# Performance work log

Measured on AMD Instinct MI355X. Metric: run time of the kernel, lower is better.

The kernel has to match this reference:

```python
import jax, jax.numpy as jnp
import numpy as np

B, S, IN = 64, 600, 3
H, C, K = 512, 80, 20
U = 64  # char_len
OUT = 1 + 6 * K


def lstm_cell(x, h, c, W_ih, W_hh, b_ih, b_hh):
    # PyTorch LSTMCell: gates order i, f, g, o
    gates = x @ W_ih.T + b_ih + h @ W_hh.T + b_hh
    i, f, g, o = jnp.split(gates, 4, axis=1)
    i = jax.nn.sigmoid(i)
    f = jax.nn.sigmoid(f)
    g = jnp.tanh(g)
    o = jax.nn.sigmoid(o)
    c_new = f * c + i * g
    h_new = o * jnp.tanh(c_new)
    return h_new, c_new


def setup_inputs() -> dict:
    key = jax.random.key(0)
    ks = jax.random.split(key, 16)
    sc = 0.05
    return {
        "x": jax.random.normal(ks[0], (B, S, IN), jnp.float32),
        "chars": jax.random.uniform(ks[1], (B, U, C), jnp.float32),
        "W_ih1": jax.random.normal(ks[2], (4 * H, IN + C), jnp.float32) * sc,
        "W_hh1": jax.random.normal(ks[3], (4 * H, H), jnp.float32) * sc,
        "b_ih1": jnp.zeros((4 * H,), jnp.float32),
        "b_hh1": jnp.zeros((4 * H,), jnp.float32),
        "W_win": jax.random.normal(ks[4], (3 * K, H), jnp.float32) * sc,
        "b_win": jnp.zeros((3 * K,), jnp.float32),
        "W_ih2": jax.random.normal(ks[5], (4 * H, IN + C), jnp.float32) * sc,
        "W_hh2": jax.random.normal(ks[6], (4 * H, H), jnp.float32) * sc,
        "b_ih2": jnp.zeros((4 * H,), jnp.float32),
        "b_hh2": jnp.zeros((4 * H,), jnp.float32),
        "W_mdn": jax.random.normal(ks[7], (OUT, H), jnp.float32) * sc,
        "b_mdn": jnp.zeros((OUT,), jnp.float32),
    }


def reference(x, chars, W_ih1, W_hh1, b_ih1, b_hh1, W_win, b_win,
              W_ih2, W_hh2, b_ih2, b_hh2, W_mdn, b_mdn):
    u = jnp.arange(U, dtype=x.dtype)[None, None, :]  # [1,1,U]

    def step(carry, pt):
        h1, c1, h2, c2, window, kappa_prev = carry
        inp1 = jnp.concatenate([pt, window], axis=1)           # [B, IN+C]
        h1, c1 = lstm_cell(inp1, h1, c1, W_ih1, W_hh1, b_ih1, b_hh1)
        # Gaussian window attention (Graves)
        wout = h1 @ W_win.T + b_win                            # [B, 3K]
        a, b_, k = jnp.split(wout, 3, axis=1)
        alpha = jnp.exp(a)[:, :, None]                         # [B,K,1]
        beta = jnp.exp(b_)[:, :, None]
        kappa = kappa_prev + jnp.exp(k)                        # [B,K]
        phi = jnp.sum(alpha * jnp.exp(-beta * (kappa[:, :, None] - u) ** 2), axis=1)  # [B,U]
        window = jnp.einsum('bu,buc->bc', phi, chars)          # [B,C]
        inp2 = jnp.concatenate([pt, window], axis=1)
        h2, c2 = lstm_cell(inp2, h2, c2, W_ih2, W_hh2, b_ih2, b_hh2)
        return (h1, c1, h2, c2, window, kappa), h2

    z = jnp.zeros((B, H), x.dtype)
    carry0 = (z, z, z, z, jnp.zeros((B, C), x.dtype), jnp.zeros((B, K), x.dtype))
    _, hs2 = jax.lax.scan(step, carry0, jnp.transpose(x, (1, 0, 2)))  # [S,B,H]
    outputs = jnp.transpose(hs2, (1, 0, 2)).reshape(-1, H)             # [B*S,H]
    mdn = outputs @ W_mdn.T + b_mdn                                     # [B*S,OUT]

    eos = jax.nn.sigmoid(mdn[:, 0]).reshape(-1, 1)
    pi, mu1, mu2, sigma1, sigma2, rho = jnp.split(mdn[:, 1:], 6, axis=1)
    pi = jax.nn.softmax(pi, axis=1)
    sigma1 = jnp.exp(sigma1)
    sigma2 = jnp.exp(sigma2)
    rho = jnp.tanh(rho)
    return eos, pi, mu1, mu2, sigma1, sigma2, rho
```

## Files before the change

### kernel.cpp

```cpp
#include <hip/hip_runtime.h>


typedef unsigned int u32;
typedef unsigned short u16;
typedef unsigned long long u64;
typedef short short8 __attribute__((ext_vector_type(8)));
typedef float floatx4 __attribute__((ext_vector_type(4)));
typedef u32 u32x4 __attribute__((ext_vector_type(4)));

#define NBLK   193
#define NGEMM  128
#define AGG_BID 192
#define NTHR   512
#define SLEN   600

#define OFF_FLAG 0ull
#define OFF_GEN  16384ull
#define OFF_H1P  32768ull
#define OFF_H2P  (OFF_H1P + 131072ull)
#define OFF_WP   (OFF_H2P + 131072ull)
#define OFF_XHI  (OFF_WP + 24576ull)
#define OFF_XLO  (OFF_XHI + 2457600ull)
#define OFF_HS2  (OFF_XLO + 2457600ull)
#define WS_NEED  (OFF_HS2 + 39321600ull)

__device__ __forceinline__ float bf2f(short h) {
  return __uint_as_float(((u32)(u16)h) << 16);
}
__device__ __forceinline__ u16 f2bf(float f) {
  u32 u = __float_as_uint(f);
  u += 0x7fffu + ((u >> 16) & 1u);
  return (u16)(u >> 16);
}
__device__ __forceinline__ float fsig(float x) { return 1.0f / (1.0f + __expf(-x)); }
__device__ __forceinline__ float ftanh_(float x) { return 2.0f / (1.0f + __expf(-2.0f * x)) - 1.0f; }

__device__ __forceinline__ float lstm_point(floatx4 g, float& c) {
  float i  = fsig(g[0]);
  float f  = fsig(g[1]);
  float gg = ftanh_(g[2]);
  float o  = fsig(g[3]);
  c = f * c + i * gg;
  return o * ftanh_(c);
}

__device__ __forceinline__ u32 pack_split(float v) {
  u32 b = __float_as_uint(v);
  float rem = v - __uint_as_float(b & 0xffff0000u);
  return (b >> 16) | ((u32)f2bf(rem) << 16);
}

__device__ __forceinline__ void st_coh(u32* p, u32 v) {
  __hip_atomic_store(p, v, __ATOMIC_RELAXED, __HIP_MEMORY_SCOPE_AGENT);
}
__device__ __forceinline__ u32 ld_coh(const u32* p) {
  return __hip_atomic_load((u32*)p, __ATOMIC_RELAXED, __HIP_MEMORY_SCOPE_AGENT);
}

__device__ __forceinline__ void ld_pk8(const u32* p, short8& hi, short8& lo) {
  u64 d0 = __hip_atomic_load((u64*)(p + 0), __ATOMIC_RELAXED, __HIP_MEMORY_SCOPE_AGENT);
  u64 d1 = __hip_atomic_load((u64*)(p + 2), __ATOMIC_RELAXED, __HIP_MEMORY_SCOPE_AGENT);
  u64 d2 = __hip_atomic_load((u64*)(p + 4), __ATOMIC_RELAXED, __HIP_MEMORY_SCOPE_AGENT);
  u64 d3 = __hip_atomic_load((u64*)(p + 6), __ATOMIC_RELAXED, __HIP_MEMORY_SCOPE_AGENT);
  u32 a0 = (u32)d0, a1 = (u32)(d0 >> 32), a2 = (u32)d1, a3 = (u32)(d1 >> 32);
  u32 a4 = (u32)d2, a5 = (u32)(d2 >> 32), a6 = (u32)d3, a7 = (u32)(d3 >> 32);
  u32x4 h, l;
  h[0] = __builtin_amdgcn_perm(a1, a0, 0x05040100u); l[0] = __builtin_amdgcn_perm(a1, a0, 0x07060302u);
  h[1] = __builtin_amdgcn_perm(a3, a2, 0x05040100u); l[1] = __builtin_amdgcn_perm(a3, a2, 0x07060302u);
  h[2] = __builtin_amdgcn_perm(a5, a4, 0x05040100u); l[2] = __builtin_amdgcn_perm(a5, a4, 0x07060302u);
  h[3] = __builtin_amdgcn_perm(a7, a6, 0x05040100u); l[3] = __builtin_amdgcn_perm(a7, a6, 0x07060302u);
  hi = __builtin_bit_cast(short8, h);
  lo = __builtin_bit_cast(short8, l);
}

__device__ __forceinline__ void sync_wait(u32* flags, u32* gen, u32 lgen, int bid) {
  if (bid == AGG_BID) {
    const int i = threadIdx.x;
    if (i < NBLK) {
      u32 sp = 0;
      while (ld_coh(&flags[i * 16]) < lgen) {
        __builtin_amdgcn_s_sleep(1);
        if (++sp > (1u << 22)) break;
      }
    }
    __syncthreads();
    if (threadIdx.x < 8) st_coh(&gen[threadIdx.x * 16], lgen);
  } else {
    if (threadIdx.x == 0) {
      u32 sp = 0;
      while (ld_coh(&gen[(bid & 7) * 16]) < lgen) {
        __builtin_amdgcn_s_sleep(2);
        if (++sp > (1u << 22)) break;
      }
    }
  }
}

__device__ __forceinline__ void sync_light(u32* flags, u32* gen, u32& lgen, int bid) {
  asm volatile("s_waitcnt vmcnt(0) lgkmcnt(0)" ::: "memory");
  __syncthreads();
  lgen++;
  if (threadIdx.x == 0) st_coh(&flags[bid * 16], lgen);
  sync_wait(flags, gen, lgen, bid);
  __syncthreads();
  asm volatile("" ::: "memory");
}

__device__ __forceinline__ void sync_full(u32* flags, u32* gen, u32& lgen, int bid) {
  __syncthreads();
  lgen++;
  if (threadIdx.x == 0) {
    __threadfence();
    st_coh(&flags[bid * 16], lgen);
  }
  sync_wait(flags, gen, lgen, bid);
  if (threadIdx.x == 0) __threadfence();
  __syncthreads();
  asm volatile("" ::: "memory");
}

__global__ void init_ws(unsigned char* ws) {
  const int gtid = blockIdx.x * 256 + threadIdx.x;
  u32* flg = (u32*)(ws + OFF_FLAG);
  for (int i = gtid; i < NBLK * 16; i += 64 * 256) flg[i] = 0u;
  u32* gn = (u32*)(ws + OFF_GEN);
  if (gtid < 128) gn[gtid] = 0u;
  u32* h2p = (u32*)(ws + OFF_H2P);
  for (int i = gtid; i < 64 * 512; i += 64 * 256) h2p[i] = 0u;
  u32* wp = (u32*)(ws + OFF_WP);
  for (int i = gtid; i < 64 * 96; i += 64 * 256) wp[i] = 0u;
}

__global__ __launch_bounds__(NTHR, 1) void rnn_kernel(
    const float* __restrict__ x, const float* __restrict__ chars,
    const float* __restrict__ Wih1, const float* __restrict__ Whh1,
    const float* __restrict__ bih1, const float* __restrict__ bhh1,
    const float* __restrict__ Wwin, const float* __restrict__ bwin,
    const float* __restrict__ Wih2, const float* __restrict__ Whh2,
    const float* __restrict__ bih2, const float* __restrict__ bhh2,
    const float* __restrict__ Wmdn, const float* __restrict__ bmdn,
    float* __restrict__ out, unsigned char* __restrict__ ws)
{
  const int bid = blockIdx.x;
  const int tid = threadIdx.x;
  const int wid = tid >> 6;
  const int lane = tid & 63;
  const int unit = wid >> 2;

  u32* flags = (u32*)(ws + OFF_FLAG);
  u32* gen   = (u32*)(ws + OFF_GEN);
  u32* h1p   = (u32*)(ws + OFF_H1P);
  u32* h2p   = (u32*)(ws + OFF_H2P);
  u32* wp    = (u32*)(ws + OFF_WP);
  u16* xhi   = (u16*)(ws + OFF_XHI);
  u16* xlo   = (u16*)(ws + OFF_XLO);
  u16* hs2   = (u16*)(ws + OFF_HS2);

  u32 lgen = 0;

  __shared__ __align__(16) u16 hifrag_s[40 * 512];
  __shared__ __align__(16) u16 lofrag_s[40 * 512];
  __shared__ __align__(16) floatx4 plds[2][256];
  __shared__ __align__(16) float chars_s[64 * 80];
  __shared__ __align__(16) float smem_f[512];
  __shared__ float wout_s[64];
  __shared__ float al_s[20], be_s[20], kp_s[20];

  for (int i = bid * NTHR + tid; i < SLEN * 64 * 32; i += NBLK * NTHR) {
    int t = i >> 11;
    int r = i & 2047;
    int bb = r >> 5, q = r & 31;
    float v = (q < 3) ? x[((size_t)bb * SLEN + t) * 3 + q] : 0.0f;
    u32 b = __float_as_uint(v);
    xhi[i] = (u16)(b >> 16);
    xlo[i] = f2bf(v - __uint_as_float(b & 0xffff0000u));
  }

  const bool isg = (bid < NGEMM);
  const bool isw = (bid >= NGEMM && bid < NGEMM + 64);

  floatx4 bs1v = {0.f,0.f,0.f,0.f}, bs2v = bs1v;
  float c1 = 0.0f, c2 = 0.0f;
  int b_row = 0, hc = 0;
  float bw = 0.0f;
  const int kg = (lane >> 4) * 8;

  if (isg) {
    b_row = 16 * (wid & 3) + (lane & 15);
    hc = 4 * bid + (lane >> 4);
    if (wid == 0) {
      const int ra = lane & 15;
      const int origA = (ra & 3) * 512 + 4 * bid + (ra >> 2);
      #pragma unroll
      for (int ks = 0; ks < 20; ++ks) {
        short8 v1h, v1l, v2h, v2l;
        #pragma unroll
        for (int j = 0; j < 8; ++j) {
          int k = 32 * ks + kg + j;
          float a1 = 0.0f, a2 = 0.0f;
          if (k < 512) {
            a1 = Whh1[(size_t)origA * 512 + k];
            a2 = Whh2[(size_t)origA * 512 + k];
          } else if (k < 592) {
            a1 = Wih1[(size_t)origA * 83 + 3 + (k - 512)];
            a2 = Wih2[(size_t)origA * 83 + 3 + (k - 512)];
          } else if (k >= 608 && k < 611) {
            a1 = Wih1[(size_t)origA * 83 + (k - 608)];
            a2 = Wih2[(size_t)origA * 83 + (k - 608)];
          }
          u32 b1 = __float_as_uint(a1), b2 = __float_as_uint(a2);
          v1h[j] = (short)(u16)(b1 >> 16);
          v2h[j] = (short)(u16)(b2 >> 16);
          v1l[j] = (short)f2bf(a1 - __uint_as_float(b1 & 0xffff0000u));
          v2l[j] = (short)f2bf(a2 - __uint_as_float(b2 & 0xffff0000u));
        }
        *(short8*)(hifrag_s + ((0 * 20 + ks) << 9) + (lane << 3)) = v1h;
        *(short8*)(hifrag_s + ((1 * 20 + ks) << 9) + (lane << 3)) = v2h;
        *(short8*)(lofrag_s + ((0 * 20 + ks) << 9) + (lane << 3)) = v1l;
        *(short8*)(lofrag_s + ((1 * 20 + ks) << 9) + (lane << 3)) = v2l;
      }
    }
    #pragma unroll
    for (int r = 0; r < 4; ++r) {
      bs1v[r] = bih1[r * 512 + hc] + bhh1[r * 512 + hc];
      bs2v[r] = bih2[r * 512 + hc] + bhh2[r * 512 + hc];
    }
  } else if (isw) {
    const int b = bid - NGEMM;
    for (int i = tid; i < 64 * 80; i += NTHR)
      chars_s[i] = chars[(size_t)b * 5120 + i];
    if (tid < 20) kp_s[tid] = 0.0f;
    if (tid < 60) bw = bwin[tid];
  }

  sync_full(flags, gen, lgen, bid);

  if (isg) {
    if (unit == 0) {
      floatx4 a = {0.f,0.f,0.f,0.f}, b = a, c = a;
      short8 xh = *(const short8*)(xhi + (size_t)b_row * 32 + kg);
      short8 xl = *(const short8*)(xlo + (size_t)b_row * 32 + kg);
      short8 ah = *(const short8*)(hifrag_s + (19 << 9) + (lane << 3));
      short8 al = *(const short8*)(lofrag_s + (19 << 9) + (lane << 3));
      a = __builtin_amdgcn_mfma_f32_16x16x32_bf16(ah, xh, a, 0, 0, 0);
      b = __builtin_amdgcn_mfma_f32_16x16x32_bf16(ah, xl, b, 0, 0, 0);
      c = __builtin_amdgcn_mfma_f32_16x16x32_bf16(al, xh, c, 0, 0, 0);
      plds[0][tid] = a + b + c;
    }
    __syncthreads();
    if (unit == 1) {
      floatx4 g = plds[0][tid - 256] + bs1v;
      float h = lstm_point(g, c1);
      st_coh(&h1p[b_row * 512 + hc], pack_split(h));
    }
  }

  sync_light(flags, gen, lgen, bid);

  for (int t = 0; t < SLEN; ++t) {
    floatx4 a1a = {0.f,0.f,0.f,0.f}, a1b = a1a, a1c = a1a;
    floatx4 a2a = {0.f,0.f,0.f,0.f}, a2b = a2a, a2c = a2a;

    if (isg) {
      if (unit == 0) {
        {
          floatx4 pa = {0.f,0.f,0.f,0.f}, pb = pa, pc = pa;
          short8 bh[8], bl[8];
          #pragma unroll
          for (int k = 0; k < 8; ++k)
            ld_pk8(h2p + b_row * 512 + k * 32 + kg, bh[k], bl[k]);
          #pragma unroll
          for (int k = 0; k < 8; ++k) {
            short8 ah = *(const short8*)(hifrag_s + ((20 + k) << 9) + (lane << 3));
            short8 al = *(const short8*)(lofrag_s + ((20 + k) << 9) + (lane << 3));
            pa = __builtin_amdgcn_mfma_f32_16x16x32_bf16(ah, bh[k], pa, 0, 0, 0);
            pb = __builtin_amdgcn_mfma_f32_16x16x32_bf16(ah, bl[k], pb, 0, 0, 0);
            pc = __builtin_amdgcn_mfma_f32_16x16x32_bf16(al, bh[k], pc, 0, 0, 0);
          }
          short8 xh = *(const short8*)(xhi + ((size_t)t * 64 + b_row) * 32 + kg);
          short8 xl = *(const short8*)(xlo + ((size_t)t * 64 + b_row) * 32 + kg);
          short8 ah = *(const short8*)(hifrag_s + ((20 + 19) << 9) + (lane << 3));
          short8 al = *(const short8*)(lofrag_s + ((20 + 19) << 9) + (lane << 3));
          pa = __builtin_amdgcn_mfma_f32_16x16x32_bf16(ah, xh, pa, 0, 0, 0);
          pb = __builtin_amdgcn_mfma_f32_16x16x32_bf16(ah, xl, pb, 0, 0, 0);
          pc = __builtin_amdgcn_mfma_f32_16x16x32_bf16(al, xh, pc, 0, 0, 0);
          plds[1][tid] = pa + pb + pc;
        }
        if (t < SLEN - 1) {
          floatx4 pa = {0.f,0.f,0.f,0.f}, pb = pa, pc = pa;
          short8 bh[8], bl[8];
          #pragma unroll
          for (int k = 0; k < 8; ++k)
            ld_pk8(h1p + b_row * 512 + k * 32 + kg, bh[k], bl[k]);
          #pragma unroll
          for (int k = 0; k < 8; ++k) {
            short8 ah = *(const short8*)(hifrag_s + (k << 9) + (lane << 3));
            short8 al = *(const short8*)(lofrag_s + (k << 9) + (lane << 3));
            pa = __builtin_amdgcn_mfma_f32_16x16x32_bf16(ah, bh[k], pa, 0, 0, 0);
            pb = __builtin_amdgcn_mfma_f32_16x16x32_bf16(ah, bl[k], pb, 0, 0, 0);
            pc = __builtin_amdgcn_mfma_f32_16x16x32_bf16(al, bh[k], pc, 0, 0, 0);
          }
          short8 xh = *(const short8*)(xhi + ((size_t)(t + 1) * 64 + b_row) * 32 + kg);
          short8 xl = *(const short8*)(xlo + ((size_t)(t + 1) * 64 + b_row) * 32 + kg);
          short8 ah = *(const short8*)(hifrag_s + (19 << 9) + (lane << 3));
          short8 al = *(const short8*)(lofrag_s + (19 << 9) + (lane << 3));
          pa = __builtin_amdgcn_mfma_f32_16x16x32_bf16(ah, xh, pa, 0, 0, 0);
          pb = __builtin_amdgcn_mfma_f32_16x16x32_bf16(ah, xl, pb, 0, 0, 0);
          pc = __builtin_amdgcn_mfma_f32_16x16x32_bf16(al, xh, pc, 0, 0, 0);
          plds[0][tid] = pa + pb + pc;
        }
      } else {
        {
          short8 bh[8], bl[8];
          #pragma unroll
          for (int k = 0; k < 8; ++k)
            ld_pk8(h2p + b_row * 512 + (8 + k) * 32 + kg, bh[k], bl[k]);
          #pragma unroll
          for (int k = 0; k < 8; ++k) {
            short8 ah = *(const short8*)(hifrag_s + ((20 + 8 + k) << 9) + (lane << 3));
            short8 al = *(const short8*)(lofrag_s + ((20 + 8 + k) << 9) + (lane << 3));
            a2a = __builtin_amdgcn_mfma_f32_16x16x32_bf16(ah, bh[k], a2a, 0, 0, 0);
            a2b = __builtin_amdgcn_mfma_f32_16x16x32_bf16(ah, bl[k], a2b, 0, 0, 0);
            a2c = __builtin_amdgcn_mfma_f32_16x16x32_bf16(al, bh[k], a2c, 0, 0, 0);
          }
        }
        if (t < SLEN - 1) {
          short8 bh[8], bl[8];
          #pragma unroll
          for (int k = 0; k < 8; ++k)
            ld_pk8(h1p + b_row * 512 + (8 + k) * 32 + kg, bh[k], bl[k]);
          #pragma unroll
          for (int k = 0; k < 8; ++k) {
            short8 ah = *(const short8*)(hifrag_s + ((8 + k) << 9) + (lane << 3));
            short8 al = *(const short8*)(lofrag_s + ((8 + k) << 9) + (lane << 3));
            a1a = __builtin_amdgcn_mfma_f32_16x16x32_bf16(ah, bh[k], a1a, 0, 0, 0);
            a1b = __builtin_amdgcn_mfma_f32_16x16x32_bf16(ah, bl[k], a1b, 0, 0, 0);
            a1c = __builtin_amdgcn_mfma_f32_16x16x32_bf16(al, bh[k], a1c, 0, 0, 0);
          }
        }
      }
    } else if (isw) {
      const int b = bid - NGEMM;
      {
        u32 p = ld_coh(&h1p[b * 512 + tid]);
        smem_f[tid] = bf2f((short)(u16)p) + bf2f((short)(u16)(p >> 16));
      }
      __syncthreads();
      const int col = tid & 63;
      const int kq  = tid >> 6;
      float p = 0.0f;
      if (col < 60) {
        const floatx4* wr = (const floatx4*)(Wwin + (size_t)col * 512 + kq * 64);
        const floatx4* hr = (const floatx4*)(smem_f + kq * 64);
        #pragma unroll
        for (int k4 = 0; k4 < 16; ++k4) {
          floatx4 wv = wr[k4];
          floatx4 hv = hr[k4];
          p = fmaf(wv[0], hv[0], p);
          p = fmaf(wv[1], hv[1], p);
          p = fmaf(wv[2], hv[2], p);
          p = fmaf(wv[3], hv[3], p);
        }
      }
      __syncthreads();
      smem_f[tid] = p;
      __syncthreads();
      if (tid < 60) {
        float s = 0.0f;
        #pragma unroll
        for (int q = 0; q < 8; ++q) s += smem_f[q * 64 + tid];
        wout_s[tid] = s + bw;
      }
      __syncthreads();
      if (tid < 20) {
        al_s[tid] = __expf(wout_s[tid]);
        be_s[tid] = __expf(wout_s[20 + tid]);
        kp_s[tid] += __expf(wout_s[40 + tid]);
      }
      __syncthreads();
      if (tid < 64) {
        float u = (float)tid;
        float ph = 0.0f;
        #pragma unroll
        for (int k = 0; k < 20; ++k) {
          float d = kp_s[k] - u;
          ph = fmaf(al_s[k], __expf(-be_s[k] * d * d), ph);
        }
        smem_f[tid] = ph;
      }
      __syncthreads();
      if (tid < 80) {
        float wv = 0.0f;
        for (int u = 0; u < 64; ++u)
          wv = fmaf(smem_f[u], chars_s[u * 80 + tid], wv);
        st_coh(&wp[b * 96 + tid], pack_split(wv));
      }
    }

    sync_light(flags, gen, lgen, bid);

    if (isg && unit == 1) {
      const int j = tid - 256;
      short8 wh0, wl0, wh1, wl1, wh2, wl2;
      ld_pk8(wp + b_row * 96 +  0 + kg, wh0, wl0);
      ld_pk8(wp + b_row * 96 + 32 + kg, wh1, wl1);
      ld_pk8(wp + b_row * 96 + 64 + kg, wh2, wl2);
      {
        short8 ah0 = *(const short8*)(hifrag_s + ((20 + 16) << 9) + (lane << 3));
        short8 ah1 = *(const short8*)(hifrag_s + ((20 + 17) << 9) + (lane << 3));
        short8 ah2 = *(const short8*)(hifrag_s + ((20 + 18) << 9) + (lane << 3));
        short8 al0 = *(const short8*)(lofrag_s + ((20 + 16) << 9) + (lane << 3));
        short8 al1 = *(const short8*)(lofrag_s + ((20 + 17) << 9) + (lane << 3));
        short8 al2 = *(const short8*)(lofrag_s + ((20 + 18) << 9) + (lane << 3));
        a2a = __builtin_amdgcn_mfma_f32_16x16x32_bf16(ah0, wh0, a2a, 0, 0, 0);
        a2b = __builtin_amdgcn_mfma_f32_16x16x32_bf16(ah0, wl0, a2b, 0, 0, 0);
        a2c = __builtin_amdgcn_mfma_f32_16x16x32_bf16(al0, wh0, a2c, 0, 0, 0);
        a2a = __builtin_amdgcn_mfma_f32_16x16x32_bf16(ah1, wh1, a2a, 0, 0, 0);
        a2b = __builtin_amdgcn_mfma_f32_16x16x32_bf16(ah1, wl1, a2b, 0, 0, 0);
        a2c = __builtin_amdgcn_mfma_f32_16x16x32_bf16(al1, wh1, a2c, 0, 0, 0);
        a2a = __builtin_amdgcn_mfma_f32_16x16x32_bf16(ah2, wh2, a2a, 0, 0, 0);
        a2b = __builtin_amdgcn_mfma_f32_16x16x32_bf16(ah2, wl2, a2b, 0, 0, 0);
        a2c = __builtin_amdgcn_mfma_f32_16x16x32_bf16(al2, wh2, a2c, 0, 0, 0);
      }
      floatx4 g2 = a2a + a2b + a2c + plds[1][j] + bs2v;
      float h2v = lstm_point(g2, c2);
      st_coh(&h2p[b_row * 512 + hc], pack_split(h2v));
      hs2[((size_t)b_row * SLEN + t) * 512 + hc] = f2bf(h2v);
      if (t < SLEN - 1) {
        short8 ah0 = *(const short8*)(hifrag_s + (16 << 9) + (lane << 3));
        short8 ah1 = *(const short8*)(hifrag_s + (17 << 9) + (lane << 3));
        short8 ah2 = *(const short8*)(hifrag_s + (18 << 9) + (lane << 3));
        short8 al0 = *(const short8*)(lofrag_s + (16 << 9) + (lane << 3));
        short8 al1 = *(const short8*)(lofrag_s + (17 << 9) + (lane << 3));
        short8 al2 = *(const short8*)(lofrag_s + (18 << 9) + (lane << 3));
        a1a = __builtin_amdgcn_mfma_f32_16x16x32_bf16(ah0, wh0, a1a, 0, 0, 0);
        a1b = __builtin_amdgcn_mfma_f32_16x16x32_bf16(ah0, wl0, a1b, 0, 0, 0);
        a1c = __builtin_amdgcn_mfma_f32_16x16x32_bf16(al0, wh0, a1c, 0, 0, 0);
        a1a = __builtin_amdgcn_mfma_f32_16x16x32_bf16(ah1, wh1, a1a, 0, 0, 0);
        a1b = __builtin_amdgcn_mfma_f32_16x16x32_bf16(ah1, wl1, a1b, 0, 0, 0);
        a1c = __builtin_amdgcn_mfma_f32_16x16x32_bf16(al1, wh1, a1c, 0, 0, 0);
        a1a = __builtin_amdgcn_mfma_f32_16x16x32_bf16(ah2, wh2, a1a, 0, 0, 0);
        a1b = __builtin_amdgcn_mfma_f32_16x16x32_bf16(ah2, wl2, a1b, 0, 0, 0);
        a1c = __builtin_amdgcn_mfma_f32_16x16x32_bf16(al2, wh2, a1c, 0, 0, 0);
        floatx4 g1 = a1a + a1b + a1c + plds[0][j] + bs1v;
        float h1v = lstm_point(g1, c1);
        st_coh(&h1p[b_row * 512 + hc], pack_split(h1v));
      }
    }

    sync_light(flags, gen, lgen, bid);
  }

  sync_full(flags, gen, lgen, bid);

  {
    const int row = bid * NTHR + tid;
    if (row < 38400) {
      const u16* hrow = hs2 + (size_t)row * 512;
      {
        float acc = bmdn[0];
        for (int k8 = 0; k8 < 512; k8 += 8) {
          short8 hv = *(const short8*)(hrow + k8);
          #pragma unroll
          for (int j = 0; j < 8; ++j) acc = fmaf(bf2f(hv[j]), Wmdn[k8 + j], acc);
        }
        out[row] = fsig(acc);
      }
      {
        float a[20];
        #pragma unroll
        for (int cc = 0; cc < 20; ++cc) a[cc] = bmdn[1 + cc];
        for (int k8 = 0; k8 < 512; k8 += 8) {
          short8 hv = *(const short8*)(hrow + k8);
          float hf[8];
          #pragma unroll
          for (int j = 0; j < 8; ++j) hf[j] = bf2f(hv[j]);
          #pragma unroll
          for (int cc = 0; cc < 20; ++cc) {
            const float* wr = Wmdn + (size_t)(1 + cc) * 512 + k8;
            #pragma unroll
            for (int j = 0; j < 8; ++j) a[cc] = fmaf(hf[j], wr[j], a[cc]);
          }
        }
        float mx = a[0];
        #pragma unroll
        for (int cc = 1; cc < 20; ++cc) mx = fmaxf(mx, a[cc]);
        float s = 0.0f;
        #pragma unroll
        for (int cc = 0; cc < 20; ++cc) { a[cc] = __expf(a[cc] - mx); s += a[cc]; }
        float inv = 1.0f / s;
        float* po = out + 38400 + (size_t)row * 20;
        #pragma unroll
        for (int cc = 0; cc < 20; ++cc) po[cc] = a[cc] * inv;
      }
      for (int grp = 1; grp <= 5; ++grp) {
        float a[20];
        #pragma unroll
        for (int cc = 0; cc < 20; ++cc) a[cc] = bmdn[1 + 20 * grp + cc];
        for (int k8 = 0; k8 < 512; k8 += 8) {
          short8 hv = *(const short8*)(hrow + k8);
          float hf[8];
          #pragma unroll
          for (int j = 0; j < 8; ++j) hf[j] = bf2f(hv[j]);
          #pragma unroll
          for (int cc = 0; cc < 20; ++cc) {
            const float* wr = Wmdn + (size_t)(1 + 20 * grp + cc) * 512 + k8;
            #pragma unroll
            for (int j = 0; j < 8; ++j) a[cc] = fmaf(hf[j], wr[j], a[cc]);
          }
        }
        float* po = out + 38400 + (size_t)grp * 768000 + (size_t)row * 20;
        if (grp == 3 || grp == 4) {
          #pragma unroll
          for (int cc = 0; cc < 20; ++cc) po[cc] = __expf(a[cc]);
        } else if (grp == 5) {
          #pragma unroll
          for (int cc = 0; cc < 20; ++cc) po[cc] = ftanh_(a[cc]);
        } else {
          #pragma unroll
          for (int cc = 0; cc < 20; ++cc) po[cc] = a[cc];
        }
      }
    }
  }
}

extern "C" void kernel_launch(void* const* d_in, const int* in_sizes, int n_in,
                              void* d_out, int out_size, void* d_ws, size_t ws_size,
                              hipStream_t stream) {
  (void)in_sizes; (void)n_in; (void)out_size;
  if (ws_size < WS_NEED) return;
  init_ws<<<dim3(64), dim3(256), 0, stream>>>((unsigned char*)d_ws);
  rnn_kernel<<<dim3(NBLK), dim3(NTHR), 0, stream>>>(
      (const float*)d_in[0],  (const float*)d_in[1],
      (const float*)d_in[2],  (const float*)d_in[3],
      (const float*)d_in[4],  (const float*)d_in[5],
      (const float*)d_in[6],  (const float*)d_in[7],
      (const float*)d_in[8],  (const float*)d_in[9],
      (const float*)d_in[10], (const float*)d_in[11],
      (const float*)d_in[12], (const float*)d_in[13],
      (float*)d_out, (unsigned char*)d_ws);
}
```

Before: 12.31 ms.

## Halve GEMM block count, doubling hidden columns per block with register-cached weights

Cuts the GEMM blocks from 128 to 64, so each block now computes 8 hidden columns, split into two groups of 4, instead of 4. The total grid drops from 193 to 129 blocks, which reduces the number of participants in each grid-wide barrier per timestep. To fit the doubled weight set, the layer-1 high-part weight fragments are held in registers per wave and the rest go into one packed LDS buffer. The cost is twice the MFMA work per block per step and higher register pressure, which could lengthen the serial critical path or lower occupancy.

```diff
diff --git a/kernel.cpp b/kernel.cpp
--- a/kernel.cpp
+++ b/kernel.cpp
@@ -8,9 +8,9 @@
 typedef float floatx4 __attribute__((ext_vector_type(4)));
 typedef u32 u32x4 __attribute__((ext_vector_type(4)));
 
-#define NBLK   193
-#define NGEMM  128
-#define AGG_BID 192
+#define NBLK   129
+#define NGEMM  64
+#define AGG_BID 128
 #define NTHR   512
 #define SLEN   600
 
@@ -23,6 +23,11 @@
 #define OFF_XLO  (OFF_XHI + 2457600ull)
 #define OFF_HS2  (OFF_XLO + 2457600ull)
 #define WS_NEED  (OFF_HS2 + 39321600ull)
+
+#define L_LO(m,ks,hcq)  ((((m)*20+(ks))*2+(hcq)) << 10)
+#define L_HI2(ks,hcq)   (81920u + ((((ks)*2+(hcq))) << 10))
+#define L_PLDS(m,hcq)   (122880u + (((m)*2+(hcq)) << 12))
+#define LDS_BYTES 139264u
 
 __device__ __forceinline__ float bf2f(short h) {
   return __uint_as_float(((u32)(u16)h) << 16);
@@ -158,13 +163,13 @@
 
   u32 lgen = 0;
 
-  __shared__ __align__(16) u16 hifrag_s[40 * 512];
-  __shared__ __align__(16) u16 lofrag_s[40 * 512];
-  __shared__ __align__(16) floatx4 plds[2][256];
-  __shared__ __align__(16) float chars_s[64 * 80];
-  __shared__ __align__(16) float smem_f[512];
-  __shared__ float wout_s[64];
-  __shared__ float al_s[20], be_s[20], kp_s[20];
+  __shared__ __align__(16) unsigned char lds_raw[LDS_BYTES];
+  float* chars_s = (float*)lds_raw;
+  float* smem_f  = (float*)(lds_raw + 20480);
+  float* wout_s  = (float*)(lds_raw + 22528);
+  float* al_s    = (float*)(lds_raw + 22784);
+  float* be_s    = (float*)(lds_raw + 22864);
+  float* kp_s    = (float*)(lds_raw + 22944);
 
   for (int i = bid * NTHR + tid; i < SLEN * 64 * 32; i += NBLK * NTHR) {
     int t = i >> 11;
@@ -179,52 +184,77 @@
   const bool isg = (bid < NGEMM);
   const bool isw = (bid >= NGEMM && bid < NGEMM + 64);
 
-  floatx4 bs1v = {0.f,0.f,0.f,0.f}, bs2v = bs1v;
-  float c1 = 0.0f, c2 = 0.0f;
-  int b_row = 0, hc = 0;
+  short8 af1h[2][11];
+  floatx4 bs1q[2] = {{0,0,0,0},{0,0,0,0}}, bs2q[2] = {{0,0,0,0},{0,0,0,0}};
+  float c1q[2] = {0.0f, 0.0f}, c2q[2] = {0.0f, 0.0f};
+  int b_row = 0;
+  int hcv[2] = {0, 0};
   float bw = 0.0f;
   const int kg = (lane >> 4) * 8;
 
   if (isg) {
     b_row = 16 * (wid & 3) + (lane & 15);
-    hc = 4 * bid + (lane >> 4);
+    hcv[0] = 8 * bid + (lane >> 4);
+    hcv[1] = 8 * bid + 4 + (lane >> 4);
+    const int ra = lane & 15;
     if (wid == 0) {
-      const int ra = lane & 15;
-      const int origA = (ra & 3) * 512 + 4 * bid + (ra >> 2);
-      #pragma unroll
-      for (int ks = 0; ks < 20; ++ks) {
-        short8 v1h, v1l, v2h, v2l;
+      #pragma unroll
+      for (int hcq = 0; hcq < 2; ++hcq) {
+        const int origA = (ra & 3) * 512 + 8 * bid + 4 * hcq + (ra >> 2);
+        #pragma unroll
+        for (int ks = 0; ks < 20; ++ks) {
+          short8 v1l, v2h, v2l;
+          #pragma unroll
+          for (int j = 0; j < 8; ++j) {
+            int k = 32 * ks + kg + j;
+            float a1 = 0.0f, a2 = 0.0f;
+            if (k < 512) {
+              a1 = Whh1[(size_t)origA * 512 + k];
+              a2 = Whh2[(size_t)origA * 512 + k];
+            } else if (k < 592) {
+              a1 = Wih1[(size_t)origA * 83 + 3 + (k - 512)];
+              a2 = Wih2[(size_t)origA * 83 + 3 + (k - 512)];
+            } else if (k >= 608 && k < 611) {
+              a1 = Wih1[(size_t)origA * 83 + (k - 608)];
+              a2 = Wih2[(size_t)origA * 83 + (k - 608)];
+            }
+            u32 b1 = __float_as_uint(a1), b2 = __float_as_uint(a2);
+            v2h[j] = (short)(u16)(b2 >> 16);
+            v1l[j] = (short)f2bf(a1 - __uint_as_float(b1 & 0xffff0000u));
+            v2l[j] = (short)f2bf(a2 - __uint_as_float(b2 & 0xffff0000u));
+          }
+          *(short8*)(lds_raw + L_HI2(ks, hcq) + (lane << 4)) = v2h;
+          *(short8*)(lds_raw + L_LO(0, ks, hcq) + (lane << 4)) = v1l;
+          *(short8*)(lds_raw + L_LO(1, ks, hcq) + (lane << 4)) = v2l;
+        }
+      }
+    }
+    #pragma unroll
+    for (int hcq = 0; hcq < 2; ++hcq) {
+      const int origA = (ra & 3) * 512 + 8 * bid + 4 * hcq + (ra >> 2);
+      #pragma unroll
+      for (int s = 0; s < 11; ++s) {
+        int ks = (unit == 0) ? ((s < 8) ? s : 19) : (8 + s);
+        short8 vh;
         #pragma unroll
         for (int j = 0; j < 8; ++j) {
           int k = 32 * ks + kg + j;
-          float a1 = 0.0f, a2 = 0.0f;
-          if (k < 512) {
-            a1 = Whh1[(size_t)origA * 512 + k];
-            a2 = Whh2[(size_t)origA * 512 + k];
-          } else if (k < 592) {
-            a1 = Wih1[(size_t)origA * 83 + 3 + (k - 512)];
-            a2 = Wih2[(size_t)origA * 83 + 3 + (k - 512)];
-          } else if (k >= 608 && k < 611) {
-            a1 = Wih1[(size_t)origA * 83 + (k - 608)];
-            a2 = Wih2[(size_t)origA * 83 + (k - 608)];
-          }
-          u32 b1 = __float_as_uint(a1), b2 = __float_as_uint(a2);
-          v1h[j] = (short)(u16)(b1 >> 16);
-          v2h[j] = (short)(u16)(b2 >> 16);
-          v1l[j] = (short)f2bf(a1 - __uint_as_float(b1 & 0xffff0000u));
-          v2l[j] = (short)f2bf(a2 - __uint_as_float(b2 & 0xffff0000u));
-        }
-        *(short8*)(hifrag_s + ((0 * 20 + ks) << 9) + (lane << 3)) = v1h;
-        *(short8*)(hifrag_s + ((1 * 20 + ks) << 9) + (lane << 3)) = v2h;
-        *(short8*)(lofrag_s + ((0 * 20 + ks) << 9) + (lane << 3)) = v1l;
-        *(short8*)(lofrag_s + ((1 * 20 + ks) << 9) + (lane << 3)) = v2l;
+          float a1 = 0.0f;
+          if (k < 512)                    a1 = Whh1[(size_t)origA * 512 + k];
+          else if (k < 592)               a1 = Wih1[(size_t)origA * 83 + 3 + (k - 512)];
+          else if (k >= 608 && k < 611)   a1 = Wih1[(size_t)origA * 83 + (k - 608)];
+          vh[j] = (short)(u16)(__float_as_uint(a1) >> 16);
+        }
+        af1h[hcq][s] = vh;
       }
     }
     #pragma unroll
-    for (int r = 0; r < 4; ++r) {
-      bs1v[r] = bih1[r * 512 + hc] + bhh1[r * 512 + hc];
-      bs2v[r] = bih2[r * 512 + hc] + bhh2[r * 512 + hc];
-    }
+    for (int hcq = 0; hcq < 2; ++hcq)
+      #pragma unroll
+      for (int r = 0; r < 4; ++r) {
+        bs1q[hcq][r] = bih1[r * 512 + hcv[hcq]] + bhh1[r * 512 + hcv[hcq]];
+        bs2q[hcq][r] = bih2[r * 512 + hcv[hcq]] + bhh2[r * 512 + hcv[hcq]];
+      }
   } else if (isw) {
     const int b = bid - NGEMM;
     for (int i = tid; i < 64 * 80; i += NTHR)
@@ -237,77 +267,95 @@
 
   if (isg) {
     if (unit == 0) {
-      floatx4 a = {0.f,0.f,0.f,0.f}, b = a, c = a;
       short8 xh = *(const short8*)(xhi + (size_t)b_row * 32 + kg);
       short8 xl = *(const short8*)(xlo + (size_t)b_row * 32 + kg);
-      short8 ah = *(const short8*)(hifrag_s + (19 << 9) + (lane << 3));
-      short8 al = *(const short8*)(lofrag_s + (19 << 9) + (lane << 3));
-      a = __builtin_amdgcn_mfma_f32_16x16x32_bf16(ah, xh, a, 0, 0, 0);
-      b = __builtin_amdgcn_mfma_f32_16x16x32_bf16(ah, xl, b, 0, 0, 0);
-      c = __builtin_amdgcn_mfma_f32_16x16x32_bf16(al, xh, c, 0, 0, 0);
-      plds[0][tid] = a + b + c;
+      #pragma unroll
+      for (int hcq = 0; hcq < 2; ++hcq) {
+        floatx4 a = {0.f,0.f,0.f,0.f}, b = a, c = a;
+        short8 ah = af1h[hcq][8];
+        short8 al = *(const short8*)(lds_raw + L_LO(0, 19, hcq) + (lane << 4));
+        a = __builtin_amdgcn_mfma_f32_16x16x32_bf16(ah, xh, a, 0, 0, 0);
+        b = __builtin_amdgcn_mfma_f32_16x16x32_bf16(ah, xl, b, 0, 0, 0);
+        c = __builtin_amdgcn_mfma_f32_16x16x32_bf16(al, xh, c, 0, 0, 0);
+        *(floatx4*)(lds_raw + L_PLDS(0, hcq) + (tid << 4)) = a + b + c;
+      }
     }
     __syncthreads();
     if (unit == 1) {
-      floatx4 g = plds[0][tid - 256] + bs1v;
-      float h = lstm_point(g, c1);
-      st_coh(&h1p[b_row * 512 + hc], pack_split(h));
+      const int j = tid & 255;
+      #pragma unroll
+      for (int hcq = 0; hcq < 2; ++hcq) {
+        floatx4 g = *(const floatx4*)(lds_raw + L_PLDS(0, hcq) + (j << 4)) + bs1q[hcq];
+        float h = lstm_point(g, c1q[hcq]);
+        st_coh(&h1p[b_row * 512 + hcv[hcq]], pack_split(h));
+      }
     }
   }
 
   sync_light(flags, gen, lgen, bid);
 
   for (int t = 0; t < SLEN; ++t) {
-    floatx4 a1a = {0.f,0.f,0.f,0.f}, a1b = a1a, a1c = a1a;
-    floatx4 a2a = {0.f,0.f,0.f,0.f}, a2b = a2a, a2c = a2a;
+    floatx4 a1[2][3], a2[2][3];
+    #pragma unroll
+    for (int hcq = 0; hcq < 2; ++hcq)
+      #pragma unroll
+      for (int m = 0; m < 3; ++m) { a1[hcq][m] = {0.f,0.f,0.f,0.f}; a2[hcq][m] = {0.f,0.f,0.f,0.f}; }
 
     if (isg) {
       if (unit == 0) {
         {
-          floatx4 pa = {0.f,0.f,0.f,0.f}, pb = pa, pc = pa;
           short8 bh[8], bl[8];
           #pragma unroll
           for (int k = 0; k < 8; ++k)
             ld_pk8(h2p + b_row * 512 + k * 32 + kg, bh[k], bl[k]);
           #pragma unroll
-          for (int k = 0; k < 8; ++k) {
-            short8 ah = *(const short8*)(hifrag_s + ((20 + k) << 9) + (lane << 3));
-            short8 al = *(const short8*)(lofrag_s + ((20 + k) << 9) + (lane << 3));
-            pa = __builtin_amdgcn_mfma_f32_16x16x32_bf16(ah, bh[k], pa, 0, 0, 0);
-            pb = __builtin_amdgcn_mfma_f32_16x16x32_bf16(ah, bl[k], pb, 0, 0, 0);
-            pc = __builtin_amdgcn_mfma_f32_16x16x32_bf16(al, bh[k], pc, 0, 0, 0);
-          }
+          for (int k = 0; k < 8; ++k)
+            #pragma unroll
+            for (int hcq = 0; hcq < 2; ++hcq) {
+              short8 ah = *(const short8*)(lds_raw + L_HI2(k, hcq) + (lane << 4));
+              short8 al = *(const short8*)(lds_raw + L_LO(1, k, hcq) + (lane << 4));
+              a2[hcq][0] = __builtin_amdgcn_mfma_f32_16x16x32_bf16(ah, bh[k], a2[hcq][0], 0, 0, 0);
+              a2[hcq][1] = __builtin_amdgcn_mfma_f32_16x16x32_bf16(ah, bl[k], a2[hcq][1], 0, 0, 0);
+              a2[hcq][2] = __builtin_amdgcn_mfma_f32_16x16x32_bf16(al, bh[k], a2[hcq][2], 0, 0, 0);
+            }
           short8 xh = *(const short8*)(xhi + ((size_t)t * 64 + b_row) * 32 + kg);
           short8 xl = *(const short8*)(xlo + ((size_t)t * 64 + b_row) * 32 + kg);
-          short8 ah = *(const short8*)(hifrag_s + ((20 + 19) << 9) + (lane << 3));
-          short8 al = *(const short8*)(lofrag_s + ((20 + 19) << 9) + (lane << 3));
-          pa = __builtin_amdgcn_mfma_f32_16x16x32_bf16(ah, xh, pa, 0, 0, 0);
-          pb = __builtin_amdgcn_mfma_f32_16x16x32_bf16(ah, xl, pb, 0, 0, 0);
-          pc = __builtin_amdgcn_mfma_f32_16x16x32_bf16(al, xh, pc, 0, 0, 0);
-          plds[1][tid] = pa + pb + pc;
+          #pragma unroll
+          for (int hcq = 0; hcq < 2; ++hcq) {
+            short8 ah = *(const short8*)(lds_raw + L_HI2(19, hcq) + (lane << 4));
+            short8 al = *(const short8*)(lds_raw + L_LO(1, 19, hcq) + (lane << 4));
+            a2[hcq][0] = __builtin_amdgcn_mfma_f32_16x16x32_bf16(ah, xh, a2[hcq][0], 0, 0, 0);
+            a2[hcq][1] = __builtin_amdgcn_mfma_f32_16x16x32_bf16(ah, xl, a2[hcq][1], 0, 0, 0);
+            a2[hcq][2] = __builtin_amdgcn_mfma_f32_16x16x32_bf16(al, xh, a2[hcq][2], 0, 0, 0);
+            *(floatx4*)(lds_raw + L_PLDS(1, hcq) + (tid << 4)) = a2[hcq][0] + a2[hcq][1] + a2[hcq][2];
+          }
         }
         if (t < SLEN - 1) {
-          floatx4 pa = {0.f,0.f,0.f,0.f}, pb = pa, pc = pa;
           short8 bh[8], bl[8];
           #pragma unroll
           for (int k = 0; k < 8; ++k)
             ld_pk8(h1p + b_row * 512 + k * 32 + kg, bh[k], bl[k]);
           #pragma unroll
-          for (int k = 0; k < 8; ++k) {
-            short8 ah = *(const short8*)(hifrag_s + (k << 9) + (lane << 3));
-            short8 al = *(const short8*)(lofrag_s + (k << 9) + (lane << 3));
-            pa = __builtin_amdgcn_mfma_f32_16x16x32_bf16(ah, bh[k], pa, 0, 0, 0);
-            pb = __builtin_amdgcn_mfma_f32_16x16x32_bf16(ah, bl[k], pb, 0, 0, 0);
-            pc = __builtin_amdgcn_mfma_f32_16x16x32_bf16(al, bh[k], pc, 0, 0, 0);
-          }
+          for (int k = 0; k < 8; ++k)
+            #pragma unroll
+            for (int hcq = 0; hcq < 2; ++hcq) {
+              short8 ah = af1h[hcq][k];
+              short8 al = *(const short8*)(lds_raw + L_LO(0, k, hcq) + (lane << 4));
+              a1[hcq][0] = __builtin_amdgcn_mfma_f32_16x16x32_bf16(ah, bh[k], a1[hcq][0], 0, 0, 0);
+              a1[hcq][1] = __builtin_amdgcn_mfma_f32_16x16x32_bf16(ah, bl[k], a1[hcq][1], 0, 0, 0);
+              a1[hcq][2] = __builtin_amdgcn_mfma_f32_16x16x32_bf16(al, bh[k], a1[hcq][2], 0, 0, 0);
+            }
           short8 xh = *(const short8*)(xhi + ((size_t)(t + 1) * 64 + b_row) * 32 + kg);
           short8 xl = *(const short8*)(xlo + ((size_t)(t + 1) * 64 + b_row) * 32 + kg);
-          short8 ah = *(const short8*)(hifrag_s + (19 << 9) + (lane << 3));
-          short8 al = *(const short8*)(lofrag_s + (19 << 9) + (lane << 3));
-          pa = __builtin_amdgcn_mfma_f32_16x16x32_bf16(ah, xh, pa, 0, 0, 0);
-          pb = __builtin_amdgcn_mfma_f32_16x16x32_bf16(ah, xl, pb, 0, 0, 0);
-          pc = __builtin_amdgcn_mfma_f32_16x16x32_bf16(al, xh, pc, 0, 0, 0);
-          plds[0][tid] = pa + pb + pc;
+          #pragma unroll
+          for (int hcq = 0; hcq < 2; ++hcq) {
+            short8 ah = af1h[hcq][8];
+            short8 al = *(const short8*)(lds_raw + L_LO(0, 19, hcq) + (lane << 4));
+            a1[hcq][0] = __builtin_amdgcn_mfma_f32_16x16x32_bf16(ah, xh, a1[hcq][0], 0, 0, 0);
+            a1[hcq][1] = __builtin_amdgcn_mfma_f32_16x16x32_bf16(ah, xl, a1[hcq][1], 0, 0, 0);
+            a1[hcq][2] = __builtin_amdgcn_mfma_f32_16x16x32_bf16(al, xh, a1[hcq][2], 0, 0, 0);
+            *(floatx4*)(lds_raw + L_PLDS(0, hcq) + (tid << 4)) = a1[hcq][0] + a1[hcq][1] + a1[hcq][2];
+          }
         }
       } else {
         {
@@ -316,13 +364,15 @@
           for (int k = 0; k < 8; ++k)
             ld_pk8(h2p + b_row * 512 + (8 + k) * 32 + kg, bh[k], bl[k]);
           #pragma unroll
-          for (int k = 0; k < 8; ++k) {
-            short8 ah = *(const short8*)(hifrag_s + ((20 + 8 + k) << 9) + (lane << 3));
-            short8 al = *(const short8*)(lofrag_s + ((20 + 8 + k) << 9) + (lane << 3));
-            a2a = __builtin_amdgcn_mfma_f32_16x16x32_bf16(ah, bh[k], a2a, 0, 0, 0);
-            a2b = __builtin_amdgcn_mfma_f32_16x16x32_bf16(ah, bl[k], a2b, 0, 0, 0);
-            a2c = __builtin_amdgcn_mfma_f32_16x16x32_bf16(al, bh[k], a2c, 0, 0, 0);
-          }
+          for (int k = 0; k < 8; ++k)
+            #pragma unroll
+            for (int hcq = 0; hcq < 2; ++hcq) {
+              short8 ah = *(const short8*)(lds_raw + L_HI2(8 + k, hcq) + (lane << 4));
+              short8 al = *(const short8*)(lds_raw + L_LO(1, 8 + k, hcq) + (lane << 4));
+              a2[hcq][0] = __builtin_amdgcn_mfma_f32_16x16x32_bf16(ah, bh[k], a2[hcq][0], 0, 0, 0);
+              a2[hcq][1] = __builtin_amdgcn_mfma_f32_16x16x32_bf16(ah, bl[k], a2[hcq][1], 0, 0, 0);
+              a2[hcq][2] = __builtin_amdgcn_mfma_f32_16x16x32_bf16(al, bh[k], a2[hcq][2], 0, 0, 0);
+            }
         }
         if (t < SLEN - 1) {
           short8 bh[8], bl[8];
@@ -330,13 +380,15 @@
           for (int k = 0; k < 8; ++k)
             ld_pk8(h1p + b_row * 512 + (8 + k) * 32 + kg, bh[k], bl[k]);
           #pragma unroll
-          for (int k = 0; k < 8; ++k) {
-            short8 ah = *(const short8*)(hifrag_s + ((8 + k) << 9) + (lane << 3));
-            short8 al = *(const short8*)(lofrag_s + ((8 + k) << 9) + (lane << 3));
-            a1a = __builtin_amdgcn_mfma_f32_16x16x32_bf16(ah, bh[k], a1a, 0, 0, 0);
-            a1b = __builtin_amdgcn_mfma_f32_16x16x32_bf16(ah, bl[k], a1b, 0, 0, 0);
-            a1c = __builtin_amdgcn_mfma_f32_16x16x32_bf16(al, bh[k], a1c, 0, 0, 0);
-          }
+          for (int k = 0; k < 8; ++k)
+            #pragma unroll
+            for (int hcq = 0; hcq < 2; ++hcq) {
+              short8 ah = af1h[hcq][k];
+              short8 al = *(const short8*)(lds_raw + L_LO(0, 8 + k, hcq) + (lane << 4));
+              a1[hcq][0] = __builtin_amdgcn_mfma_f32_16x16x32_bf16(ah, bh[k], a1[hcq][0], 0, 0, 0);
+              a1[hcq][1] = __builtin_amdgcn_mfma_f32_16x16x32_bf16(ah, bl[k], a1[hcq][1], 0, 0, 0);
+              a1[hcq][2] = __builtin_amdgcn_mfma_f32_16x16x32_bf16(al, bh[k], a1[hcq][2], 0, 0, 0);
+            }
         }
       }
     } else if (isw) {
@@ -400,51 +452,47 @@
     sync_light(flags, gen, lgen, bid);
 
     if (isg && unit == 1) {
-      const int j = tid - 256;
-      short8 wh0, wl0, wh1, wl1, wh2, wl2;
-      ld_pk8(wp + b_row * 96 +  0 + kg, wh0, wl0);
-      ld_pk8(wp + b_row * 96 + 32 + kg, wh1, wl1);
-      ld_pk8(wp + b_row * 96 + 64 + kg, wh2, wl2);
-      {
-        short8 ah0 = *(const short8*)(hifrag_s + ((20 + 16) << 9) + (lane << 3));
-        short8 ah1 = *(const short8*)(hifrag_s + ((20 + 17) << 9) + (lane << 3));
-        short8 ah2 = *(const short8*)(hifrag_s + ((20 + 18) << 9) + (lane << 3));
-        short8 al0 = *(const short8*)(lofrag_s + ((20 + 16) << 9) + (lane << 3));
-        short8 al1 = *(const short8*)(lofrag_s + ((20 + 17) << 9) + (lane << 3));
-        short8 al2 = *(const short8*)(lofrag_s + ((20 + 18) << 9) + (lane << 3));
-        a2a = __builtin_amdgcn_mfma_f32_16x16x32_bf16(ah0, wh0, a2a, 0, 0, 0);
-        a2b = __builtin_amdgcn_mfma_f32_16x16x32_bf16(ah0, wl0, a2b, 0, 0, 0);
-        a2c = __builtin_amdgcn_mfma_f32_16x16x32_bf16(al0, wh0, a2c, 0, 0, 0);
-        a2a = __builtin_amdgcn_mfma_f32_16x16x32_bf16(ah1, wh1, a2a, 0, 0, 0);
-        a2b = __builtin_amdgcn_mfma_f32_16x16x32_bf16(ah1, wl1, a2b, 0, 0, 0);
-        a2c = __builtin_amdgcn_mfma_f32_16x16x32_bf16(al1, wh1, a2c, 0, 0, 0);
-        a2a = __builtin_amdgcn_mfma_f32_16x16x32_bf16(ah2, wh2, a2a, 0, 0, 0);
-        a2b = __builtin_amdgcn_mfma_f32_16x16x32_bf16(ah2, wl2, a2b, 0, 0, 0);
-        a2c = __builtin_amdgcn_mfma_f32_16x16x32_bf16(al2, wh2, a2c, 0, 0, 0);
-      }
-      floatx4 g2 = a2a + a2b + a2c + plds[1][j] + bs2v;
-      float h2v = lstm_point(g2, c2);
-      st_coh(&h2p[b_row * 512 + hc], pack_split(h2v));
-      hs2[((size_t)b_row * SLEN + t) * 512 + hc] = f2bf(h2v);
+      const int j = tid & 255;
+      short8 wh[3], wl[3];
+      ld_pk8(wp + b_row * 96 +  0 + kg, wh[0], wl[0]);
+      ld_pk8(wp + b_row * 96 + 32 + kg, wh[1], wl[1]);
+      ld_pk8(wp + b_row * 96 + 64 + kg, wh[2], wl[2]);
+      #pragma unroll
+      for (int jj = 0; jj < 3; ++jj)
+        #pragma unroll
+        for (int hcq = 0; hcq < 2; ++hcq) {
+          short8 ah = *(const short8*)(lds_raw + L_HI2(16 + jj, hcq) + (lane << 4));
+          short8 al = *(const short8*)(lds_raw + L_LO(1, 16 + jj, hcq) + (lane << 4));
+          a2[hcq][0] = __builtin_amdgcn_mfma_f32_16x16x32_bf16(ah, wh[jj], a2[hcq][0], 0, 0, 0);
+          a2[hcq][1] = __builtin_amdgcn_mfma_f32_16x16x32_bf16(ah, wl[jj], a2[hcq][1], 0, 0, 0);
+          a2[hcq][2] = __builtin_amdgcn_mfma_f32_16x16x32_bf16(al, wh[jj], a2[hcq][2], 0, 0, 0);
+        }
+      #pragma unroll
+      for (int hcq = 0; hcq < 2; ++hcq) {
+        floatx4 g2 = a2[hcq][0] + a2[hcq][1] + a2[hcq][2]
+                   + *(const floatx4*)(lds_raw + L_PLDS(1, hcq) + (j << 4)) + bs2q[hcq];
+        float h2v = lstm_point(g2, c2q[hcq]);
+        st_coh(&h2p[b_row * 512 + hcv[hcq]], pack_split(h2v));
+        hs2[((size_t)b_row * SLEN + t) * 512 + hcv[hcq]] = f2bf(h2v);
+      }
       if (t < SLEN - 1) {
-        short8 ah0 = *(const short8*)(hifrag_s + (16 << 9) + (lane << 3));
-        short8 ah1 = *(const short8*)(hifrag_s + (17 << 9) + (lane << 3));
-        short8 ah2 = *(const short8*)(hifrag_s + (18 << 9) + (lane << 3));
-        short8 al0 = *(const short8*)(lofrag_s + (16 << 9) + (lane << 3));
-        short8 al1 = *(const short8*)(lofrag_s + (17 << 9) + (lane << 3));
-        short8 al2 = *(const short8*)(lofrag_s + (18 << 9) + (lane << 3));
-        a1a = __builtin_amdgcn_mfma_f32_16x16x32_bf16(ah0, wh0, a1a, 0, 0, 0);
-        a1b = __builtin_amdgcn_mfma_f32_16x16x32_bf16(ah0, wl0, a1b, 0, 0, 0);
-        a1c = __builtin_amdgcn_mfma_f32_16x16x32_bf16(al0, wh0, a1c, 0, 0, 0);
-        a1a = __builtin_amdgcn_mfma_f32_16x16x32_bf16(ah1, wh1, a1a, 0, 0, 0);
-        a1b = __builtin_amdgcn_mfma_f32_16x16x32_bf16(ah1, wl1, a1b, 0, 0, 0);
-        a1c = __builtin_amdgcn_mfma_f32_16x16x32_bf16(al1, wh1, a1c, 0, 0, 0);
-        a1a = __builtin_amdgcn_mfma_f32_16x16x32_bf16(ah2, wh2, a1a, 0, 0, 0);
-        a1b = __builtin_amdgcn_mfma_f32_16x16x32_bf16(ah2, wl2, a1b, 0, 0, 0);
-        a1c = __builtin_amdgcn_mfma_f32_16x16x32_bf16(al2, wh2, a1c, 0, 0, 0);
-        floatx4 g1 = a1a + a1b + a1c + plds[0][j] + bs1v;
-        float h1v = lstm_point(g1, c1);
-        st_coh(&h1p[b_row * 512 + hc], pack_split(h1v));
+        #pragma unroll
+        for (int jj = 0; jj < 3; ++jj)
+          #pragma unroll
+          for (int hcq = 0; hcq < 2; ++hcq) {
+            short8 ah = af1h[hcq][8 + jj];
+            short8 al = *(const short8*)(lds_raw + L_LO(0, 16 + jj, hcq) + (lane << 4));
+            a1[hcq][0] = __builtin_amdgcn_mfma_f32_16x16x32_bf16(ah, wh[jj], a1[hcq][0], 0, 0, 0);
+            a1[hcq][1] = __builtin_amdgcn_mfma_f32_16x16x32_bf16(ah, wl[jj], a1[hcq][1], 0, 0, 0);
+            a1[hcq][2] = __builtin_amdgcn_mfma_f32_16x16x32_bf16(al, wh[jj], a1[hcq][2], 0, 0, 0);
+          }
+        #pragma unroll
+        for (int hcq = 0; hcq < 2; ++hcq) {
+          floatx4 g1 = a1[hcq][0] + a1[hcq][1] + a1[hcq][2]
+                     + *(const floatx4*)(lds_raw + L_PLDS(0, hcq) + (j << 4)) + bs1q[hcq];
+          float h1v = lstm_point(g1, c1q[hcq]);
+          st_coh(&h1p[b_row * 512 + hcv[hcq]], pack_split(h1v));
+        }
       }
     }
 
```

Measured after the change: 13.37 ms. +8.5%, slower.
